# Kernel tuning notes

Hardware: AMD Instinct MI355X
Metric: run time of the kernel (lower is better)

Reference implementation:

```python
import jax, jax.numpy as jnp
import numpy as np

KEY_DIM, VALUE_DIM, NUM_HEAD, OUT_DIM = 128, 64, 4, 64
HEAD_KDIM = KEY_DIM // NUM_HEAD   # 32
HEAD_VDIM = VALUE_DIM // NUM_HEAD # 16

def _xavier(key, shape):
    # xavier_uniform over (fan_in=shape[0], fan_out=prod(shape[1:])) like torch
    fan_in, fan_out = shape[0], int(np.prod(shape[1:]))
    lim = float(np.sqrt(6.0 / (fan_in + fan_out)))
    return jax.random.uniform(key, shape, jnp.float32, -lim, lim)

def setup_inputs() -> dict:
    key = jax.random.key(0)
    ks = jax.random.split(key, 7)
    B, Q, K = 2, 4096, 4096
    return {
        "q_data": jax.random.normal(ks[0], (B, Q, KEY_DIM), jnp.float32),
        "m_data": jax.random.normal(ks[1], (B, K, VALUE_DIM), jnp.float32),
        "mask": jax.random.randint(ks[2], (B, K), 0, 2, jnp.int32),
        "q_weights": _xavier(ks[3], (KEY_DIM, NUM_HEAD, HEAD_KDIM)),
        "k_weights": _xavier(ks[4], (VALUE_DIM, NUM_HEAD, HEAD_KDIM)),
        "v_weights": _xavier(ks[5], (VALUE_DIM, NUM_HEAD, HEAD_VDIM)),
        "o_weights": _xavier(ks[6], (NUM_HEAD, HEAD_VDIM, OUT_DIM)),
        "o_bias": jnp.zeros((OUT_DIM,), jnp.float32),
    }

def reference(q_data, m_data, mask, q_weights, k_weights, v_weights, o_weights, o_bias):
    head_kdim = q_weights.shape[-1]
    scale = head_kdim ** (-0.5)
    Q = jnp.einsum('bqa,ahc->bqhc', q_data, q_weights) * scale
    K = jnp.einsum('bka,ahc->bkhc', m_data, k_weights)
    V = jnp.einsum('bka,ahc->bkhc', m_data, v_weights)
    logits = jnp.einsum('bqhc,bkhc->bhqk', Q, K)
    neg = jnp.finfo(logits.dtype).min
    logits = jnp.where(mask[:, None, None, :] == 0, neg, logits)
    weights = jax.nn.softmax(logits, axis=-1)
    weight_avg = jnp.einsum('bhqk,bkhc->bqhc', weights, V)
    return jnp.einsum('bqhc,hco->bqo', weight_avg, o_weights) + o_bias
```

## Files before the change

kernel.cpp:

```cpp
#include <hip/hip_runtime.h>
#include <stdint.h>

#define B_  2
#define QN  4096
#define KN  4096
#define AD  128
#define MD  64
#define H_  4
#define C_  32
#define CV  16
#define OD  64

typedef short bf16x8 __attribute__((ext_vector_type(8)));
typedef short bf16x4 __attribute__((ext_vector_type(4)));
typedef float f32x4  __attribute__((ext_vector_type(4)));

__device__ __forceinline__ short f2bf(float f) {
  union { float f; unsigned u; } v; v.f = f;
  unsigned r = v.u + 0x7fffu + ((v.u >> 16) & 1u);
  return (short)(r >> 16);
}
__device__ __forceinline__ float bf2f(short s) {
  union { unsigned u; float f; } v; v.u = ((unsigned)(unsigned short)s) << 16;
  return v.f;
}
__device__ __forceinline__ unsigned pack2t(float a, float b) {
  union { float f; unsigned u; } ua, ub; ua.f = a; ub.f = b;
  return __builtin_amdgcn_perm(ub.u, ua.u, 0x07060302u);
}
__device__ __forceinline__ bf16x4 pack4t(f32x4 p) {
  union { unsigned u[2]; bf16x4 v; } t;
  t.u[0] = pack2t(p[0], p[1]); t.u[1] = pack2t(p[2], p[3]);
  return t.v;
}

__global__ __launch_bounds__(256) void k_pre(const float* __restrict__ qd, const float* __restrict__ md,
                                             const float* __restrict__ qw, const float* __restrict__ kw,
                                             const float* __restrict__ vw, const int* __restrict__ mask,
                                             short* __restrict__ canon, int* __restrict__ idx,
                                             int* __restrict__ kc) {
  __shared__ int wcnt[64];
  __shared__ int wbase[64];
  const int bid = blockIdx.x;
  if (bid < 782) {
    const int i8 = (bid*256 + threadIdx.x) * 8;
    const float* src; int off;
    if      (i8 < 1048576) { src = qd; off = i8; }
    else if (i8 < 1572864) { src = md; off = i8 - 1048576; }
    else if (i8 < 1589248) { src = qw; off = i8 - 1572864; }
    else if (i8 < 1597440) { src = kw; off = i8 - 1589248; }
    else                   { src = vw; off = i8 - 1597440; }
    const f32x4 a = *(const f32x4*)(src + off);
    const f32x4 b = *(const f32x4*)(src + off + 4);
    bf16x8 o;
    o[0]=f2bf(a[0]); o[1]=f2bf(a[1]); o[2]=f2bf(a[2]); o[3]=f2bf(a[3]);
    o[4]=f2bf(b[0]); o[5]=f2bf(b[1]); o[6]=f2bf(b[2]); o[7]=f2bf(b[3]);
    *(bf16x8*)(canon + i8) = o;
    return;
  }
  const int b = bid - 782;
  const int lane = threadIdx.x & 63, wid = threadIdx.x >> 6;
  unsigned long long bals[16];
  #pragma unroll
  for (int p = 0; p < 16; ++p) {
    const int seg = wid*16 + p;
    const int m = mask[b*KN + seg*64 + lane] != 0;
    bals[p] = __ballot(m);
    if (lane == 0) wcnt[seg] = __popcll(bals[p]);
  }
  __syncthreads();
  if (wid == 0) {
    int v = wcnt[lane]; int incl = v;
    for (int d = 1; d < 64; d <<= 1) { int o = __shfl_up(incl, d); if (lane >= d) incl += o; }
    wbase[lane] = incl - v;
    if (lane == 63) kc[b] = incl;
  }
  __syncthreads();
  #pragma unroll
  for (int p = 0; p < 16; ++p) {
    const int seg = wid*16 + p;
    if ((bals[p] >> lane) & 1ull) {
      const int pos = __popcll(bals[p] & ((1ull << lane) - 1ull));
      idx[b*KN + wbase[seg] + pos] = seg*64 + lane;
    }
  }
}

__global__ __launch_bounds__(256) void k_proj(const short* __restrict__ qdc, const short* __restrict__ mdc,
                                              const short* __restrict__ qwc, const short* __restrict__ kwc,
                                              const short* __restrict__ vwc,
                                              const int* __restrict__ idx, const int* __restrict__ kc,
                                              short* __restrict__ Qp, short* __restrict__ Kp,
                                              short* __restrict__ Vpt) {
  const int lane = threadIdx.x & 63;
  const int n = lane & 15, quad = lane >> 4;
  const f32x4 z4 = {0.f,0.f,0.f,0.f};
  if (blockIdx.x < 1024) {
    const int t = blockIdx.x*4 + (threadIdx.x >> 6);
    const int rt = t >> 3, ct = t & 7;
    const int row = rt*16 + n;
    const int hc0 = ct*16;
    f32x4 acc = z4;
    #pragma unroll
    for (int ak = 0; ak < 4; ++ak) {
      const int a0 = ak*32 + quad*8;
      bf16x8 afrag = *(const bf16x8*)(qdc + row*AD + a0);
      bf16x8 bfrag;
      #pragma unroll
      for (int j = 0; j < 8; ++j) bfrag[j] = qwc[(a0 + j)*128 + hc0 + n];
      acc = __builtin_amdgcn_mfma_f32_16x16x32_bf16(afrag, bfrag, acc, 0, 0, 0);
    }
    const int h = hc0 >> 5, c0 = (hc0 & 31) + n;
    const float s = 0.17677669529663687f * 1.44269504088896341f;
    #pragma unroll
    for (int r = 0; r < 4; ++r) {
      const int rr = rt*16 + quad*4 + r;
      const int bb = rr >> 12, q = rr & 4095;
      Qp[((bb*H_ + h)*QN + q)*C_ + c0] = f2bf(acc[r] * s);
    }
    return;
  }
  const int t = (blockIdx.x - 1024)*4 + (threadIdx.x >> 6);
  const int b = t / 3072; const int rem = t - b*3072;
  const int rt = rem / 12, ct = rem - rt*12;
  const int Kc = kc[b];
  const int nch = (Kc + 31) >> 5;
  if (rt*16 >= nch*32) return;
  const int j = rt*16 + n;
  const int valid = (j < Kc);
  const int src = valid ? idx[b*KN + j] : 0;
  const short* mrow = mdc + (b*KN + src)*MD;
  const int hc = ct*16 + n;
  f32x4 acc = z4;
  #pragma unroll
  for (int ch = 0; ch < 2; ++ch) {
    const int a0 = ch*32 + quad*8;
    bf16x8 afrag = *(const bf16x8*)(mrow + a0);
    if (!valid) {
      #pragma unroll
      for (int jj = 0; jj < 8; ++jj) afrag[jj] = 0;
    }
    bf16x8 bfrag;
    if (ct < 8) {
      #pragma unroll
      for (int jj = 0; jj < 8; ++jj) bfrag[jj] = kwc[(a0 + jj)*128 + hc];
    } else {
      #pragma unroll
      for (int jj = 0; jj < 8; ++jj) bfrag[jj] = vwc[(a0 + jj)*64 + hc - 128];
    }
    acc = __builtin_amdgcn_mfma_f32_16x16x32_bf16(afrag, bfrag, acc, 0, 0, 0);
  }
  if (ct < 8) {
    const int h = hc >> 5, c = hc & 31;
    #pragma unroll
    for (int r = 0; r < 4; ++r) {
      const int jj2 = rt*16 + quad*4 + r;
      Kp[((b*H_ + h)*KN + jj2)*C_ + c] = f2bf(acc[r]);
    }
  } else {
    const int hc2 = hc - 128; const int h = hc2 >> 4, cv = hc2 & 15;
    bf16x4 pk; pk[0]=f2bf(acc[0]); pk[1]=f2bf(acc[1]); pk[2]=f2bf(acc[2]); pk[3]=f2bf(acc[3]);
    *(bf16x4*)(Vpt + ((b*H_ + h)*CV + cv)*KN + rt*16 + quad*4) = pk;
  }
}

__global__ __launch_bounds__(256) void k_attn(const short* __restrict__ Qp, const short* __restrict__ Kp,
                                              const short* __restrict__ Vpt, const int* __restrict__ kc,
                                              float* __restrict__ Onum, float* __restrict__ Lsum) {
  __shared__ short P_lds[4][32*40];
  const int lane = threadIdx.x & 63, wid = threadIdx.x >> 6;
  const int gid = blockIdx.x;
  const int split = gid & 1;
  const int h = (gid >> 1) & 3;
  const int qblk = (gid >> 3) & 31;
  const int b = gid >> 8;
  const int qt = qblk*128 + wid*32;
  const int bh = b*H_ + h;
  const int n = lane & 15, quad = lane >> 4;
  const short* Qb = Qp + (bh*QN + qt)*C_;
  const short* Kb = Kp + bh*KN*C_;
  const short* Vb = Vpt + bh*CV*KN;
  const bf16x8 qb0 = *(const bf16x8*)(Qb + n*C_ + quad*8);
  const bf16x8 qb1 = *(const bf16x8*)(Qb + (16 + n)*C_ + quad*8);
  const int Kc = kc[b];
  const int nch = (Kc + 31) >> 5;
  const f32x4 z4 = {0.f,0.f,0.f,0.f};
  f32x4 o0 = z4, o1 = z4;
  float l0 = 0.f, l1 = 0.f;
  short* Pw = &P_lds[wid][0];
  bf16x8 kf0, kf1, va;
  int ci = split;
  if (ci < nch) {
    const int kb = ci*32;
    kf0 = *(const bf16x8*)(Kb + (kb + n)*C_ + quad*8);
    kf1 = *(const bf16x8*)(Kb + (kb + 16 + n)*C_ + quad*8);
    va  = *(const bf16x8*)(Vb + n*KN + kb + quad*8);
  }
  for (; ci < nch; ci += 2) {
    const bf16x8 ckf0 = kf0, ckf1 = kf1, cva = va;
    const int cin = ci + 2;
    if (cin < nch) {
      const int kb2 = cin*32;
      kf0 = *(const bf16x8*)(Kb + (kb2 + n)*C_ + quad*8);
      kf1 = *(const bf16x8*)(Kb + (kb2 + 16 + n)*C_ + quad*8);
      va  = *(const bf16x8*)(Vb + n*KN + kb2 + quad*8);
    }
    f32x4 s00 = __builtin_amdgcn_mfma_f32_16x16x32_bf16(ckf0, qb0, z4, 0, 0, 0);
    f32x4 s01 = __builtin_amdgcn_mfma_f32_16x16x32_bf16(ckf0, qb1, z4, 0, 0, 0);
    f32x4 s10 = __builtin_amdgcn_mfma_f32_16x16x32_bf16(ckf1, qb0, z4, 0, 0, 0);
    f32x4 s11 = __builtin_amdgcn_mfma_f32_16x16x32_bf16(ckf1, qb1, z4, 0, 0, 0);
    f32x4 p00, p01, p10, p11;
    #pragma unroll
    for (int r = 0; r < 4; ++r) {
      p00[r] = __builtin_amdgcn_exp2f(s00[r]);
      p01[r] = __builtin_amdgcn_exp2f(s01[r]);
      p10[r] = __builtin_amdgcn_exp2f(s10[r]);
      p11[r] = __builtin_amdgcn_exp2f(s11[r]);
    }
    l0 += ((p00[0]+p00[1])+(p00[2]+p00[3])) + ((p10[0]+p10[1])+(p10[2]+p10[3]));
    l1 += ((p01[0]+p01[1])+(p01[2]+p01[3])) + ((p11[0]+p11[1])+(p11[2]+p11[3]));
    *(bf16x4*)(Pw + n*40 + quad*4)           = pack4t(p00);
    *(bf16x4*)(Pw + n*40 + 16 + quad*4)      = pack4t(p10);
    *(bf16x4*)(Pw + (16+n)*40 + quad*4)      = pack4t(p01);
    *(bf16x4*)(Pw + (16+n)*40 + 16 + quad*4) = pack4t(p11);
    const bf16x8 pb0 = *(const bf16x8*)(Pw + n*40 + quad*8);
    const bf16x8 pb1 = *(const bf16x8*)(Pw + (16+n)*40 + quad*8);
    o0 = __builtin_amdgcn_mfma_f32_16x16x32_bf16(cva, pb0, o0, 0, 0, 0);
    o1 = __builtin_amdgcn_mfma_f32_16x16x32_bf16(cva, pb1, o1, 0, 0, 0);
  }
  l0 += __shfl_xor(l0, 16); l0 += __shfl_xor(l0, 32);
  l1 += __shfl_xor(l1, 16); l1 += __shfl_xor(l1, 32);
  if (lane < 16) {
    float* Lrow = Lsum + ((split*B_ + b)*H_ + h)*QN + qt;
    Lrow[lane] = l0; Lrow[16 + lane] = l1;
  }
  float* On = Onum + (split*B_ + b)*QN*64;
  #pragma unroll
  for (int r = 0; r < 4; ++r) {
    const int cv = quad*4 + r;
    On[(qt + n)*64 + h*16 + cv]      = o0[r];
    On[(qt + 16 + n)*64 + h*16 + cv] = o1[r];
  }
}

__global__ __launch_bounds__(256) void k_out(const float* __restrict__ Onum, const float* __restrict__ Lsum,
                                             const int* __restrict__ kc,
                                             const float* __restrict__ owf, const float* __restrict__ obf,
                                             float* __restrict__ out) {
  const int t = blockIdx.x*4 + (threadIdx.x >> 6);
  const int lane = threadIdx.x & 63;
  const int rt = t >> 2, ct = t & 3;
  const int n = lane & 15, quad = lane >> 4;
  const int row = rt*16 + n;
  const int b = row >> 12;
  const int q = row & 4095;
  const int Kc = kc[b]; const int nch = (Kc + 31) >> 5;
  const float npad = (float)(nch*32 - Kc);
  const float* O0 = Onum;
  const float* O1 = Onum + B_*QN*64;
  const float* L0 = Lsum;
  const float* L1 = Lsum + B_*H_*QN;
  const int o0c = ct*16;
  const f32x4 z4 = {0.f,0.f,0.f,0.f};
  f32x4 acc = z4;
  #pragma unroll
  for (int ch = 0; ch < 2; ++ch) {
    const int hcb = ch*32 + quad*8;
    const int h = hcb >> 4;
    const float l = L0[(b*H_ + h)*QN + q] + L1[(b*H_ + h)*QN + q] - npad;
    const float inv = 1.00135f / fmaxf(l, 1e-20f);
    const float* orow0 = O0 + row*64 + hcb;
    const float* orow1 = O1 + row*64 + hcb;
    bf16x8 afrag;
    #pragma unroll
    for (int jj = 0; jj < 8; ++jj) afrag[jj] = f2bf((orow0[jj] + orow1[jj]) * inv);
    bf16x8 bfrag;
    #pragma unroll
    for (int jj = 0; jj < 8; ++jj) bfrag[jj] = f2bf(owf[(hcb + jj)*64 + o0c + n]);
    acc = __builtin_amdgcn_mfma_f32_16x16x32_bf16(afrag, bfrag, acc, 0, 0, 0);
  }
  const float bias = obf[o0c + n];
  #pragma unroll
  for (int r = 0; r < 4; ++r) {
    const int rr = rt*16 + quad*4 + r;
    out[rr*64 + o0c + n] = acc[r] + bias;
  }
}

extern "C" void kernel_launch(void* const* d_in, const int* in_sizes, int n_in,
                              void* d_out, int out_size, void* d_ws, size_t ws_size,
                              hipStream_t stream) {
  const float* qd  = (const float*)d_in[0];
  const float* md  = (const float*)d_in[1];
  const int*   msk = (const int*)  d_in[2];
  const float* qw  = (const float*)d_in[3];
  const float* kw  = (const float*)d_in[4];
  const float* vw  = (const float*)d_in[5];
  const float* ow  = (const float*)d_in[6];
  const float* ob  = (const float*)d_in[7];
  float* out = (float*)d_out;

  char* ws = (char*)d_ws;
  int*   idx   = (int*)  (ws);
  int*   kc    = (int*)  (ws + (32<<10));
  short* canon = (short*)(ws + (64<<10));
  short* qdc = canon;
  short* mdc = canon + 1048576;
  short* qwc = canon + 1572864;
  short* kwc = canon + 1589248;
  short* vwc = canon + 1597440;
  short* Qp   = (short*)(ws + (64<<10) + (4u<<20));
  short* Kp   = (short*)(ws + (64<<10) + (6u<<20));
  short* Vpt  = (short*)(ws + (64<<10) + (8u<<20));
  float* Onum = (float*)(ws + (64<<10) + (9u<<20));
  float* Lsum = (float*)(ws + (64<<10) + (13u<<20));

  hipLaunchKernelGGL(k_pre,  dim3(784),  dim3(256), 0, stream, qd, md, qw, kw, vw, msk, canon, idx, kc);
  hipLaunchKernelGGL(k_proj, dim3(2560), dim3(256), 0, stream, qdc, mdc, qwc, kwc, vwc, idx, kc, Qp, Kp, Vpt);
  hipLaunchKernelGGL(k_attn, dim3(512),  dim3(256), 0, stream, Qp, Kp, Vpt, kc, Onum, Lsum);
  hipLaunchKernelGGL(k_out,  dim3(512),  dim3(256), 0, stream, Onum, Lsum, kc, ow, ob, out);
}
```

Measured before the change: 108.9 us.

## Fuse bf16 conversion into projection and output projection into attention

The separate fp32-to-bf16 canonicalization pass is dropped. Projection now reads fp32 inputs and weights directly and converts them in registers, so k_pre shrinks to a small mask-compaction kernel. The attention kernel now runs 512 threads, with the 8 waves covering 4 heads and 2 key splits for one 32-query tile. It merges the splits through LDS, normalizes, and performs the output projection plus bias in place, which removes the Onum/Lsum global round trip and the k_out launch. The trade-offs are half as many attention blocks (256), larger LDS per block, and redundant weight conversions in every projection wave.

```diff
diff --git a/kernel.cpp b/kernel.cpp
--- a/kernel.cpp
+++ b/kernel.cpp
@@ -20,10 +20,6 @@
   unsigned r = v.u + 0x7fffu + ((v.u >> 16) & 1u);
   return (short)(r >> 16);
 }
-__device__ __forceinline__ float bf2f(short s) {
-  union { unsigned u; float f; } v; v.u = ((unsigned)(unsigned short)s) << 16;
-  return v.f;
-}
 __device__ __forceinline__ unsigned pack2t(float a, float b) {
   union { float f; unsigned u; } ua, ub; ua.f = a; ub.f = b;
   return __builtin_amdgcn_perm(ub.u, ua.u, 0x07060302u);
@@ -33,32 +29,18 @@
   t.u[0] = pack2t(p[0], p[1]); t.u[1] = pack2t(p[2], p[3]);
   return t.v;
 }
-
-__global__ __launch_bounds__(256) void k_pre(const float* __restrict__ qd, const float* __restrict__ md,
-                                             const float* __restrict__ qw, const float* __restrict__ kw,
-                                             const float* __restrict__ vw, const int* __restrict__ mask,
-                                             short* __restrict__ canon, int* __restrict__ idx,
-                                             int* __restrict__ kc) {
+__device__ __forceinline__ bf16x8 cvt8(f32x4 a, f32x4 b) {
+  bf16x8 o;
+  o[0]=f2bf(a[0]); o[1]=f2bf(a[1]); o[2]=f2bf(a[2]); o[3]=f2bf(a[3]);
+  o[4]=f2bf(b[0]); o[5]=f2bf(b[1]); o[6]=f2bf(b[2]); o[7]=f2bf(b[3]);
+  return o;
+}
+
+__global__ __launch_bounds__(256) void k_compact(const int* __restrict__ mask,
+                                                 int* __restrict__ idx, int* __restrict__ kc) {
   __shared__ int wcnt[64];
   __shared__ int wbase[64];
-  const int bid = blockIdx.x;
-  if (bid < 782) {
-    const int i8 = (bid*256 + threadIdx.x) * 8;
-    const float* src; int off;
-    if      (i8 < 1048576) { src = qd; off = i8; }
-    else if (i8 < 1572864) { src = md; off = i8 - 1048576; }
-    else if (i8 < 1589248) { src = qw; off = i8 - 1572864; }
-    else if (i8 < 1597440) { src = kw; off = i8 - 1589248; }
-    else                   { src = vw; off = i8 - 1597440; }
-    const f32x4 a = *(const f32x4*)(src + off);
-    const f32x4 b = *(const f32x4*)(src + off + 4);
-    bf16x8 o;
-    o[0]=f2bf(a[0]); o[1]=f2bf(a[1]); o[2]=f2bf(a[2]); o[3]=f2bf(a[3]);
-    o[4]=f2bf(b[0]); o[5]=f2bf(b[1]); o[6]=f2bf(b[2]); o[7]=f2bf(b[3]);
-    *(bf16x8*)(canon + i8) = o;
-    return;
-  }
-  const int b = bid - 782;
+  const int b = blockIdx.x;
   const int lane = threadIdx.x & 63, wid = threadIdx.x >> 6;
   unsigned long long bals[16];
   #pragma unroll
@@ -86,9 +68,9 @@
   }
 }
 
-__global__ __launch_bounds__(256) void k_proj(const short* __restrict__ qdc, const short* __restrict__ mdc,
-                                              const short* __restrict__ qwc, const short* __restrict__ kwc,
-                                              const short* __restrict__ vwc,
+__global__ __launch_bounds__(256) void k_proj(const float* __restrict__ qdf, const float* __restrict__ mdf,
+                                              const float* __restrict__ qwf, const float* __restrict__ kwf,
+                                              const float* __restrict__ vwf,
                                               const int* __restrict__ idx, const int* __restrict__ kc,
                                               short* __restrict__ Qp, short* __restrict__ Kp,
                                               short* __restrict__ Vpt) {
@@ -104,10 +86,11 @@
     #pragma unroll
     for (int ak = 0; ak < 4; ++ak) {
       const int a0 = ak*32 + quad*8;
-      bf16x8 afrag = *(const bf16x8*)(qdc + row*AD + a0);
+      const float* ap = qdf + row*AD + a0;
+      bf16x8 afrag = cvt8(*(const f32x4*)ap, *(const f32x4*)(ap + 4));
       bf16x8 bfrag;
       #pragma unroll
-      for (int j = 0; j < 8; ++j) bfrag[j] = qwc[(a0 + j)*128 + hc0 + n];
+      for (int j = 0; j < 8; ++j) bfrag[j] = f2bf(qwf[(a0 + j)*128 + hc0 + n]);
       acc = __builtin_amdgcn_mfma_f32_16x16x32_bf16(afrag, bfrag, acc, 0, 0, 0);
     }
     const int h = hc0 >> 5, c0 = (hc0 & 31) + n;
@@ -129,13 +112,13 @@
   const int j = rt*16 + n;
   const int valid = (j < Kc);
   const int src = valid ? idx[b*KN + j] : 0;
-  const short* mrow = mdc + (b*KN + src)*MD;
+  const float* mrow = mdf + (b*KN + src)*MD;
   const int hc = ct*16 + n;
   f32x4 acc = z4;
   #pragma unroll
   for (int ch = 0; ch < 2; ++ch) {
     const int a0 = ch*32 + quad*8;
-    bf16x8 afrag = *(const bf16x8*)(mrow + a0);
+    bf16x8 afrag = cvt8(*(const f32x4*)(mrow + a0), *(const f32x4*)(mrow + a0 + 4));
     if (!valid) {
       #pragma unroll
       for (int jj = 0; jj < 8; ++jj) afrag[jj] = 0;
@@ -143,10 +126,10 @@
     bf16x8 bfrag;
     if (ct < 8) {
       #pragma unroll
-      for (int jj = 0; jj < 8; ++jj) bfrag[jj] = kwc[(a0 + jj)*128 + hc];
+      for (int jj = 0; jj < 8; ++jj) bfrag[jj] = f2bf(kwf[(a0 + jj)*128 + hc]);
     } else {
       #pragma unroll
-      for (int jj = 0; jj < 8; ++jj) bfrag[jj] = vwc[(a0 + jj)*64 + hc - 128];
+      for (int jj = 0; jj < 8; ++jj) bfrag[jj] = f2bf(vwf[(a0 + jj)*64 + hc - 128]);
     }
     acc = __builtin_amdgcn_mfma_f32_16x16x32_bf16(afrag, bfrag, acc, 0, 0, 0);
   }
@@ -164,17 +147,18 @@
   }
 }
 
-__global__ __launch_bounds__(256) void k_attn(const short* __restrict__ Qp, const short* __restrict__ Kp,
+__global__ __launch_bounds__(512) void k_attn(const short* __restrict__ Qp, const short* __restrict__ Kp,
                                               const short* __restrict__ Vpt, const int* __restrict__ kc,
-                                              float* __restrict__ Onum, float* __restrict__ Lsum) {
-  __shared__ short P_lds[4][32*40];
+                                              const float* __restrict__ w2f, const float* __restrict__ obf,
+                                              float* __restrict__ out) {
+  __shared__ short P_lds[8][32*40];
+  __shared__ float Of[2][32*65];
+  __shared__ float Lb[2*4*32];
+  __shared__ short ObfA[32*72];
   const int lane = threadIdx.x & 63, wid = threadIdx.x >> 6;
-  const int gid = blockIdx.x;
-  const int split = gid & 1;
-  const int h = (gid >> 1) & 3;
-  const int qblk = (gid >> 3) & 31;
-  const int b = gid >> 8;
-  const int qt = qblk*128 + wid*32;
+  const int h = wid & 3, split = wid >> 2;
+  const int flatq = blockIdx.x * 32;
+  const int b = flatq >> 12, qt = flatq & 4095;
   const int bh = b*H_ + h;
   const int n = lane & 15, quad = lane >> 4;
   const short* Qb = Qp + (bh*QN + qt)*C_;
@@ -228,62 +212,52 @@
     o0 = __builtin_amdgcn_mfma_f32_16x16x32_bf16(cva, pb0, o0, 0, 0, 0);
     o1 = __builtin_amdgcn_mfma_f32_16x16x32_bf16(cva, pb1, o1, 0, 0, 0);
   }
+  #pragma unroll
+  for (int r = 0; r < 4; ++r) {
+    const int hc = h*16 + quad*4 + r;
+    Of[split][n*65 + hc]      = o0[r];
+    Of[split][(16+n)*65 + hc] = o1[r];
+  }
   l0 += __shfl_xor(l0, 16); l0 += __shfl_xor(l0, 32);
   l1 += __shfl_xor(l1, 16); l1 += __shfl_xor(l1, 32);
   if (lane < 16) {
-    float* Lrow = Lsum + ((split*B_ + b)*H_ + h)*QN + qt;
-    Lrow[lane] = l0; Lrow[16 + lane] = l1;
-  }
-  float* On = Onum + (split*B_ + b)*QN*64;
-  #pragma unroll
-  for (int r = 0; r < 4; ++r) {
-    const int cv = quad*4 + r;
-    On[(qt + n)*64 + h*16 + cv]      = o0[r];
-    On[(qt + 16 + n)*64 + h*16 + cv] = o1[r];
-  }
-}
-
-__global__ __launch_bounds__(256) void k_out(const float* __restrict__ Onum, const float* __restrict__ Lsum,
-                                             const int* __restrict__ kc,
-                                             const float* __restrict__ owf, const float* __restrict__ obf,
-                                             float* __restrict__ out) {
-  const int t = blockIdx.x*4 + (threadIdx.x >> 6);
-  const int lane = threadIdx.x & 63;
-  const int rt = t >> 2, ct = t & 3;
-  const int n = lane & 15, quad = lane >> 4;
-  const int row = rt*16 + n;
-  const int b = row >> 12;
-  const int q = row & 4095;
-  const int Kc = kc[b]; const int nch = (Kc + 31) >> 5;
-  const float npad = (float)(nch*32 - Kc);
-  const float* O0 = Onum;
-  const float* O1 = Onum + B_*QN*64;
-  const float* L0 = Lsum;
-  const float* L1 = Lsum + B_*H_*QN;
-  const int o0c = ct*16;
-  const f32x4 z4 = {0.f,0.f,0.f,0.f};
-  f32x4 acc = z4;
-  #pragma unroll
-  for (int ch = 0; ch < 2; ++ch) {
-    const int hcb = ch*32 + quad*8;
-    const int h = hcb >> 4;
-    const float l = L0[(b*H_ + h)*QN + q] + L1[(b*H_ + h)*QN + q] - npad;
-    const float inv = 1.00135f / fmaxf(l, 1e-20f);
-    const float* orow0 = O0 + row*64 + hcb;
-    const float* orow1 = O1 + row*64 + hcb;
-    bf16x8 afrag;
-    #pragma unroll
-    for (int jj = 0; jj < 8; ++jj) afrag[jj] = f2bf((orow0[jj] + orow1[jj]) * inv);
-    bf16x8 bfrag;
-    #pragma unroll
-    for (int jj = 0; jj < 8; ++jj) bfrag[jj] = f2bf(owf[(hcb + jj)*64 + o0c + n]);
-    acc = __builtin_amdgcn_mfma_f32_16x16x32_bf16(afrag, bfrag, acc, 0, 0, 0);
-  }
-  const float bias = obf[o0c + n];
-  #pragma unroll
-  for (int r = 0; r < 4; ++r) {
-    const int rr = rt*16 + quad*4 + r;
-    out[rr*64 + o0c + n] = acc[r] + bias;
+    Lb[split*128 + h*32 + lane]      = l0;
+    Lb[split*128 + h*32 + 16 + lane] = l1;
+  }
+  __syncthreads();
+  {
+    const float npad = (float)(nch*32 - Kc);
+    const int e = threadIdx.x * 4;
+    const int q = e >> 6, hc = e & 63;
+    const int hh = hc >> 4;
+    const float l = Lb[hh*32 + q] + Lb[128 + hh*32 + q] - npad;
+    const float inv = 1.00135f / l;
+    bf16x4 pk;
+    #pragma unroll
+    for (int jj = 0; jj < 4; ++jj)
+      pk[jj] = f2bf((Of[0][q*65 + hc + jj] + Of[1][q*65 + hc + jj]) * inv);
+    *(bf16x4*)(ObfA + q*72 + hc) = pk;
+  }
+  __syncthreads();
+  {
+    const int mt = wid & 1, nt = wid >> 1;
+    f32x4 acc = z4;
+    #pragma unroll
+    for (int kchunk = 0; kchunk < 2; ++kchunk) {
+      const bf16x8 afrag = *(const bf16x8*)(ObfA + (mt*16 + n)*72 + kchunk*32 + quad*8);
+      bf16x8 bfrag;
+      #pragma unroll
+      for (int jj = 0; jj < 8; ++jj)
+        bfrag[jj] = f2bf(w2f[(kchunk*32 + quad*8 + jj)*64 + nt*16 + n]);
+      acc = __builtin_amdgcn_mfma_f32_16x16x32_bf16(afrag, bfrag, acc, 0, 0, 0);
+    }
+    const int ocol = nt*16 + n;
+    const float bias = obf[ocol];
+    #pragma unroll
+    for (int r = 0; r < 4; ++r) {
+      const int qg = flatq + mt*16 + quad*4 + r;
+      out[qg*64 + ocol] = acc[r] + bias;
+    }
   }
 }
 
@@ -301,22 +275,13 @@
   float* out = (float*)d_out;
 
   char* ws = (char*)d_ws;
-  int*   idx   = (int*)  (ws);
-  int*   kc    = (int*)  (ws + (32<<10));
-  short* canon = (short*)(ws + (64<<10));
-  short* qdc = canon;
-  short* mdc = canon + 1048576;
-  short* qwc = canon + 1572864;
-  short* kwc = canon + 1589248;
-  short* vwc = canon + 1597440;
-  short* Qp   = (short*)(ws + (64<<10) + (4u<<20));
-  short* Kp   = (short*)(ws + (64<<10) + (6u<<20));
-  short* Vpt  = (short*)(ws + (64<<10) + (8u<<20));
-  float* Onum = (float*)(ws + (64<<10) + (9u<<20));
-  float* Lsum = (float*)(ws + (64<<10) + (13u<<20));
-
-  hipLaunchKernelGGL(k_pre,  dim3(784),  dim3(256), 0, stream, qd, md, qw, kw, vw, msk, canon, idx, kc);
-  hipLaunchKernelGGL(k_proj, dim3(2560), dim3(256), 0, stream, qdc, mdc, qwc, kwc, vwc, idx, kc, Qp, Kp, Vpt);
-  hipLaunchKernelGGL(k_attn, dim3(512),  dim3(256), 0, stream, Qp, Kp, Vpt, kc, Onum, Lsum);
-  hipLaunchKernelGGL(k_out,  dim3(512),  dim3(256), 0, stream, Onum, Lsum, kc, ow, ob, out);
-}
+  int*   idx = (int*)  (ws);
+  int*   kc  = (int*)  (ws + (32<<10));
+  short* Qp  = (short*)(ws + (64<<10));
+  short* Kp  = (short*)(ws + (64<<10) + (2u<<20));
+  short* Vpt = (short*)(ws + (64<<10) + (4u<<20));
+
+  hipLaunchKernelGGL(k_compact, dim3(2),    dim3(256), 0, stream, msk, idx, kc);
+  hipLaunchKernelGGL(k_proj,    dim3(2560), dim3(256), 0, stream, qd, md, qw, kw, vw, idx, kc, Qp, Kp, Vpt);
+  hipLaunchKernelGGL(k_attn,    dim3(256),  dim3(512), 0, stream, Qp, Kp, Vpt, kc, ow, ob, out);
+}
```

New measurement: 108.2 us. Within noise of the previous version (-0.7%).
